# Performance work log

Measured on AMD Instinct MI355X. Metric: run time of the kernel, lower is better.

The kernel has to match this reference:

```python
import jax, jax.numpy as jnp
import numpy as np

B = 8; DIM = 384; H = 8; DH = 48; T = 256; T2 = 64; DEPTH = 4; P = 14; G = 16
SCALE = DIM ** -0.5
BN_INV = 1.0 / float(np.sqrt(1.0 + 1e-5))

def _gelu(x):
    return jax.nn.gelu(x, approximate=False)

def _ln(x, g, b):
    m = x.mean(-1, keepdims=True)
    v = ((x - m) ** 2).mean(-1, keepdims=True)
    return (x - m) / jnp.sqrt(v + 1e-5) * g + b

def _conv(x, w, bi, s, p, groups=1):
    y = jax.lax.conv_general_dilated(x, w, (s, s), [(p, p), (p, p)],
        dimension_numbers=('NCHW', 'OIHW', 'NCHW'), feature_group_count=groups)
    return y + bi[None, :, None, None]

def _gumbel_softmax(logits, key, tau=1.0):
    g = jax.random.gumbel(key, logits.shape, logits.dtype)
    return jax.nn.softmax((logits + g) / tau, axis=-1)

def setup_inputs() -> dict:
    key = jax.random.key(0)
    ks = jax.random.split(key, 20)
    def n(k, shape, s=0.02):
        return jax.random.normal(k, shape, jnp.float32) * s
    D = DEPTH
    return {
        'img': jax.random.normal(ks[0], (B, 3, 224, 224), jnp.float32),
        'adj': jax.random.randint(ks[1], (T, T), 0, 2).astype(jnp.int32),
        'ln_g': jnp.ones((D, DIM), jnp.float32), 'ln_b': jnp.zeros((D, DIM), jnp.float32),
        'gcn_wq': n(ks[2], (D, DH, DH)), 'gcn_wk': n(ks[3], (D, DH, DH)), 'gcn_wv': n(ks[4], (D, DH, DH)),
        'wq': n(ks[5], (D, DIM, DIM)), 'wk': n(ks[6], (D, DIM, DIM)), 'wv': n(ks[7], (D, DIM, DIM)),
        'w_kf': n(ks[8], (D, 2 * DIM, H)), 'w_kf2': n(ks[9], (D, H, T)), 'w_kf3': n(ks[10], (D, H, T2)),
        'sD': jnp.ones((D, H, T), jnp.float32), 'sD2': jnp.ones((D, H, T2), jnp.float32),
        'randmat': n(ks[11], (D, H, H), 1.0),
        'conv1_w': n(ks[12], (DIM, 3, 3, 3), 0.05), 'conv1_b': jnp.zeros((DIM,), jnp.float32),
        'bn_g': jnp.ones((DIM,), jnp.float32), 'bn_b': jnp.zeros((DIM,), jnp.float32),
        'conv2_w': n(ks[13], (DIM, 1, 3, 3), 0.05), 'conv2_b': jnp.zeros((DIM,), jnp.float32),
        'emb_w': n(ks[14], (4 * DIM, DIM)), 'emb_b': jnp.zeros((DIM,), jnp.float32),
        'upool_w': n(ks[15], (DIM, T2)), 'upool_b': jnp.zeros((T2,), jnp.float32),
        'upoolout_w': n(ks[16], (DIM, 1)), 'upoolout_b': jnp.zeros((1,), jnp.float32),
    }

def _forward(img, adj, ln_g, ln_b, gcn_wq, gcn_wk, gcn_wv, wq, wk, wv,
             w_kf, w_kf2, w_kf3, sD, sD2, randmat,
             conv1_w, conv1_b, bn_g, bn_b, conv2_w, conv2_b, emb_w, emb_b,
             upool_w, upool_b, upoolout_w, upoolout_b):
    b = img.shape[0]
    # patchify: (b,3,224,224) -> (b*256, 3, 14, 14)
    x = img.reshape(b, 3, G, P, G, P).transpose(0, 2, 4, 1, 3, 5).reshape(b * G * G, 3, P, P)
    y = _conv(x, conv1_w, conv1_b, 2, 1)                       # (b*256,384,7,7)
    y = y * BN_INV * bn_g[None, :, None, None] + bn_b[None, :, None, None]  # BN eval (mean=0,var=1)
    y = _gelu(y)
    y = _conv(y, conv2_w, conv2_b, 2, 1, groups=DIM)           # depthwise -> (b*256,384,4,4)
    y = y.reshape(b * G * G, DIM, 2, 2, 2, 2).max(axis=(3, 5)) # adaptive max pool -> 2x2
    y = y.reshape(b, G * G, DIM * 4)                           # (b,256, c*p1*p2)
    x = y @ emb_w + emb_b                                      # (b,256,384)
    rep_adj = jnp.broadcast_to(adj.astype(jnp.float32)[None, None], (b, H, T, T))

    def attention(xn, adjbh, i, label):
        t = xn.shape[1]
        x4 = xn.reshape(b, t, H, DH).transpose(0, 2, 1, 3)     # b h t d
        q4 = jnp.einsum('bhts,bhsd->bhtd', adjbh, x4 @ gcn_wq[i])  # GCN: A @ (X W)
        k4 = jnp.einsum('bhts,bhsd->bhtd', adjbh, x4 @ gcn_wk[i])
        q = q4.transpose(0, 2, 1, 3).reshape(b, t, DIM) @ wq[i]
        k = k4.transpose(0, 2, 1, 3).reshape(b, t, DIM) @ wk[i]
        rm0 = _gelu(jnp.concatenate([q, k], -1) @ w_kf[i])     # (b,t,h)
        rm = jnp.einsum('bth,btg->bhg', rm0, rm0)
        if label == 0:
            rmd = jax.nn.sigmoid((rm @ w_kf2[i]) / sD[i])      # (b,h,t)
        else:
            rmd = jax.nn.sigmoid((rm @ w_kf3[i]) / sD2[i])
        qh = q.reshape(b, t, H, DH).transpose(0, 2, 1, 3)
        kh = k.reshape(b, t, H, DH).transpose(0, 2, 1, 3)
        score = jnp.einsum('bhld,bhtd->bhlt', qh, kh) * SCALE
        score = jax.nn.leaky_relu(score)
        score = rmd[:, :, :, None] * score * rmd[:, :, None, :]   # diag_embed(rmd) @ S @ diag_embed(rmd)
        score = jnp.einsum('lh,bhk->blk', randmat[i], score.reshape(b, H, t * t)).reshape(b, H, t, t)
        score = jnp.where(adjbh > 0, score, -1e12)
        attn = jax.nn.softmax(score, axis=-1)
        v4 = jnp.einsum('bhts,bhsd->bhtd', attn, x4 @ gcn_wv[i])  # attn weights as edge weights
        return _gelu(v4.transpose(0, 2, 1, 3).reshape(b, t, DIM) @ wv[i])

    kg = jax.random.key(42)
    for i in range(DEPTH):
        xn = _ln(x, ln_g[i], ln_b[i])
        if i < DEPTH // 2:
            x = attention(xn, rep_adj, i, 0) + x
        else:
            if i == DEPTH // 2:
                tmp = (x @ upool_w + upool_b).transpose(0, 2, 1)       # (b,64,256)
                tmp = _gumbel_softmax(tmp, jax.random.fold_in(kg, i))
                x = tmp @ x                                            # (b,64,384)
                rep_adj = jnp.einsum('bls,bhst->bhlt', tmp, rep_adj)   # C A C^T
                rep_adj = jnp.einsum('bhlt,bmt->bhlm', rep_adj, tmp)
                xn = _ln(x, ln_g[i], ln_b[i])
            x = attention(xn, rep_adj, i, 1) + x

    tmp = (x @ upoolout_w + upoolout_b).transpose(0, 2, 1)             # (b,1,64)
    tmp = _gumbel_softmax(tmp, jax.random.fold_in(kg, 99))
    return tmp @ x                                                     # (b,1,384)

def reference(img, adj, ln_g, ln_b, gcn_wq, gcn_wk, gcn_wv, wq, wk, wv,
              w_kf, w_kf2, w_kf3, sD, sD2, randmat,
              conv1_w, conv1_b, bn_g, bn_b, conv2_w, conv2_b, emb_w, emb_b,
              upool_w, upool_b, upoolout_w, upoolout_b):
    return _forward(img, adj, ln_g, ln_b, gcn_wq, gcn_wk, gcn_wv, wq, wk, wv,
                    w_kf, w_kf2, w_kf3, sD, sD2, randmat,
                    conv1_w, conv1_b, bn_g, bn_b, conv2_w, conv2_b, emb_w, emb_b,
                    upool_w, upool_b, upoolout_w, upoolout_b)
```

## Files before the change

kernel.cpp:

```cpp
#include <hip/hip_runtime.h>
#include <stdint.h>
#include <math.h>

#define NB 8
#define NDIM 384
#define NHD 8
#define DHD 48

__device__ float g_patch[2048 * 1536];
__device__ float g_x[NB * 256 * NDIM];
__device__ float g_xb[NB * 64 * NDIM];
__device__ float g_xq[NB * NHD * 256 * DHD];
__device__ float g_xk[NB * NHD * 256 * DHD];
__device__ float g_xv[NB * NHD * 256 * DHD];
__device__ float g_q4[NB * 256 * NDIM];
__device__ float g_k4[NB * 256 * NDIM];
__device__ float g_q[NB * 256 * NDIM];
__device__ float g_k[NB * 256 * NDIM];
__device__ float g_rm0[NB * 256 * NHD];
__device__ float g_rmd[NB * NHD * 256];
__device__ float g_score[NB * NHD * 256 * 256];
__device__ float g_score2[NB * NHD * 256 * 256];
__device__ float g_logits[NB * 256 * 64];
__device__ float g_tmp[NB * 64 * 256];
__device__ float g_e1[NB * 64 * 256];
__device__ float g_adj2[NB * 64 * 64];

__device__ __forceinline__ float* dev_buf(int s) {
  switch (s) {
    case 0: return g_patch;
    case 1: return g_x;
    case 2: return g_q4;
    case 3: return g_k4;
    case 4: return g_q;
    case 5: return g_k;
    case 6: return g_logits;
    default: return nullptr;
  }
}
#define SEL_PATCH 0
#define SEL_X 1
#define SEL_Q4 2
#define SEL_K4 3
#define SEL_Q 4
#define SEL_K 5
#define SEL_LOGITS 6

__device__ __forceinline__ float gelu_f(float x) {
  return 0.5f * x * (1.0f + erff(x * 0.70710678118654752440f));
}

__host__ __device__ inline void threefry2x32(uint32_t k0, uint32_t k1,
                                             uint32_t x0, uint32_t x1,
                                             uint32_t* o0, uint32_t* o1) {
  uint32_t ks2 = k0 ^ k1 ^ 0x1BD11BDAu;
#define TF_R(r) { x0 += x1; x1 = (x1 << (r)) | (x1 >> (32 - (r))); x1 ^= x0; }
  x0 += k0; x1 += k1;
  TF_R(13) TF_R(15) TF_R(26) TF_R(6)
  x0 += k1; x1 += ks2 + 1u;
  TF_R(17) TF_R(29) TF_R(16) TF_R(24)
  x0 += ks2; x1 += k0 + 2u;
  TF_R(13) TF_R(15) TF_R(26) TF_R(6)
  x0 += k0; x1 += k1 + 3u;
  TF_R(17) TF_R(29) TF_R(16) TF_R(24)
  x0 += k1; x1 += ks2 + 4u;
  TF_R(13) TF_R(15) TF_R(26) TF_R(6)
  x0 += ks2; x1 += k0 + 5u;
#undef TF_R
  *o0 = x0; *o1 = x1;
}

__device__ __forceinline__ double gumbel_from(uint32_t k0, uint32_t k1,
                                              uint32_t idx) {
  uint32_t o0, o1;
  threefry2x32(k0, k1, 0u, idx, &o0, &o1);
  uint32_t bits = o0 ^ o1;
  uint32_t ub = (bits >> 9) | 0x3f800000u;
  float f = __uint_as_float(ub) - 1.0f;
  const float tiny = 1.17549435e-38f;
  float u = fmaxf(f + tiny, tiny);
  return -log(-log((double)u));
}

__global__ __launch_bounds__(256) void k_patch(const float* __restrict__ img,
                                               const float* __restrict__ w1, const float* __restrict__ b1,
                                               const float* __restrict__ bng, const float* __restrict__ bnb,
                                               const float* __restrict__ w2, const float* __restrict__ b2) {
  __shared__ float s_in[3 * 256];
  __shared__ float s_c1[96 * 49];
  __shared__ __align__(16) float s_w1t[27 * 96];
  const float BN_INV = (float)0.99999500003749968752;
  int p = blockIdx.x >> 2;
  int chunk = blockIdx.x & 3;
  int obase = chunk * 96;
  int b = p >> 8, g = p & 255, gi = g >> 4, gj = g & 15;
  int tid = threadIdx.x;
  for (int idx = tid; idx < 3 * 256; idx += 256) {
    int c = idx >> 8, r = idx & 255, py = r >> 4, px = r & 15;
    float v = 0.f;
    if (py >= 1 && py <= 14 && px >= 1 && px <= 14)
      v = img[(((size_t)b * 3 + c) * 224 + gi * 14 + py - 1) * 224 + gj * 14 + px - 1];
    s_in[idx] = v;
  }
  for (int i = tid; i < 27 * 96; i += 256) {
    int j = i / 96, ch = i - j * 96;
    s_w1t[i] = w1[(size_t)(obase + ch) * 27 + j];
  }
  __syncthreads();
  int wave = tid >> 6, lane = tid & 63;
  int y = lane / 7, x = lane - y * 7;
  bool act = lane < 49;
  float in[27];
#pragma unroll
  for (int c = 0; c < 3; ++c)
#pragma unroll
    for (int ky = 0; ky < 3; ++ky)
#pragma unroll
      for (int kx = 0; kx < 3; ++kx)
        in[c * 9 + ky * 3 + kx] = act ? s_in[c * 256 + (2 * y + ky) * 16 + (2 * x + kx)] : 0.f;

  for (int ci = 0; ci < 24; ci += 4) {
    int cl0 = wave * 24 + ci;
    int o0 = obase + cl0;
    float a0 = b1[o0], a1 = b1[o0 + 1], a2 = b1[o0 + 2], a3 = b1[o0 + 3];
#pragma unroll
    for (int j = 0; j < 27; ++j) {
      float4 w = *(const float4*)&s_w1t[j * 96 + cl0];
      float ij = in[j];
      a0 += ij * w.x;
      a1 += ij * w.y;
      a2 += ij * w.z;
      a3 += ij * w.w;
    }
    a0 = a0 * BN_INV * bng[o0] + bnb[o0];
    a1 = a1 * BN_INV * bng[o0 + 1] + bnb[o0 + 1];
    a2 = a2 * BN_INV * bng[o0 + 2] + bnb[o0 + 2];
    a3 = a3 * BN_INV * bng[o0 + 3] + bnb[o0 + 3];
    if (act) {
      s_c1[cl0 * 49 + lane] = gelu_f(a0);
      s_c1[(cl0 + 1) * 49 + lane] = gelu_f(a1);
      s_c1[(cl0 + 2) * 49 + lane] = gelu_f(a2);
      s_c1[(cl0 + 3) * 49 + lane] = gelu_f(a3);
    }
  }
  __syncthreads();
  if (tid < 96) {
    int cl = tid, c = obase + cl;
    float wd[9];
#pragma unroll
    for (int j = 0; j < 9; ++j) wd[j] = w2[c * 9 + j];
    float bb2 = b2[c];
    const float* sc = &s_c1[cl * 49];
    float o2[4][4];
#pragma unroll
    for (int yy = 0; yy < 4; ++yy)
#pragma unroll
      for (int xx = 0; xx < 4; ++xx) {
        float a = bb2;
#pragma unroll
        for (int ky = 0; ky < 3; ++ky) {
          int iy = 2 * yy + ky - 1;
          if (iy < 0 || iy >= 7) continue;
#pragma unroll
          for (int kx = 0; kx < 3; ++kx) {
            int ix = 2 * xx + kx - 1;
            if (ix < 0 || ix >= 7) continue;
            a += sc[iy * 7 + ix] * wd[ky * 3 + kx];
          }
        }
        o2[yy][xx] = a;
      }
    float4 r;
    r.x = fmaxf(fmaxf(o2[0][0], o2[0][1]), fmaxf(o2[1][0], o2[1][1]));
    r.y = fmaxf(fmaxf(o2[0][2], o2[0][3]), fmaxf(o2[1][2], o2[1][3]));
    r.z = fmaxf(fmaxf(o2[2][0], o2[2][1]), fmaxf(o2[3][0], o2[3][1]));
    r.w = fmaxf(fmaxf(o2[2][2], o2[2][3]), fmaxf(o2[3][2], o2[3][3]));
    *(float4*)&g_patch[(size_t)p * 1536 + c * 4] = r;
  }
}

template <int RPB>
__global__ void k_gemm(const float* __restrict__ W, const float* __restrict__ bias,
                       int selA, int selC, int selR,
                       int M, int K, int N, int act) {
  extern __shared__ float sA[];
  const float* A = dev_buf(selA);
  float* C = dev_buf(selC);
  const float* R = (selR >= 0) ? dev_buf(selR) : nullptr;
  int tid = threadIdx.x;
  int bs = blockDim.x;
  int r0 = blockIdx.x * RPB;
  float acc[RPB];
#pragma unroll
  for (int r = 0; r < RPB; ++r) acc[r] = 0.0f;
  const float4 z4 = {0.f, 0.f, 0.f, 0.f};
  for (int k0 = 0; k0 < K; k0 += 384) {
    __syncthreads();
    for (int idx = tid; idx < RPB * 96; idx += bs) {
      int r = idx / 96, q = idx - r * 96;
      int m = r0 + r;
      ((float4*)sA)[idx] = (m < M) ? ((const float4*)(A + (size_t)m * K + k0))[q] : z4;
    }
    __syncthreads();
    const float* Wp = W + (size_t)k0 * N + tid;
    float w0 = Wp[0], w1 = Wp[N], w2 = Wp[2 * (size_t)N], w3 = Wp[3 * (size_t)N];
#pragma unroll 2
    for (int k = 0; k < 384; k += 4) {
      float n0 = 0.f, n1 = 0.f, n2 = 0.f, n3 = 0.f;
      if (k + 4 < 384) {
        const float* Wn = Wp + (size_t)(k + 4) * N;
        n0 = Wn[0]; n1 = Wn[N]; n2 = Wn[2 * (size_t)N]; n3 = Wn[3 * (size_t)N];
      }
#pragma unroll
      for (int r = 0; r < RPB; ++r) {
        float4 a = *(const float4*)&sA[r * 384 + k];
        acc[r] += a.x * w0 + a.y * w1 + a.z * w2 + a.w * w3;
      }
      w0 = n0; w1 = n1; w2 = n2; w3 = n3;
    }
  }
#pragma unroll
  for (int r = 0; r < RPB; ++r) {
    int m = r0 + r;
    if (m >= M) break;
    float v = acc[r];
    if (bias) v += bias[tid];
    if (act == 1) v = gelu_f(v);
    if (R) v += R[(size_t)m * N + tid];
    C[(size_t)m * N + tid] = v;
  }
}

__global__ __launch_bounds__(384) void k_gemm_sk(const float* __restrict__ W, int M, int K, int N) {
  __shared__ float sA[8 * 384];
  int mb = M >> 3;
  int kc = blockIdx.x / mb;
  int rb = blockIdx.x - kc * mb;
  int r0 = rb << 3;
  int k0 = kc * 384;
  int tid = threadIdx.x;
  float acc[8];
#pragma unroll
  for (int r = 0; r < 8; ++r) acc[r] = 0.0f;
  for (int idx = tid; idx < 8 * 96; idx += 384) {
    int r = idx / 96, q = idx - r * 96;
    ((float4*)sA)[idx] = ((const float4*)(g_patch + (size_t)(r0 + r) * K + k0))[q];
  }
  __syncthreads();
  const float* Wp = W + (size_t)k0 * N + tid;
  float w0 = Wp[0], w1 = Wp[N], w2 = Wp[2 * (size_t)N], w3 = Wp[3 * (size_t)N];
#pragma unroll 2
  for (int k = 0; k < 384; k += 4) {
    float n0 = 0.f, n1 = 0.f, n2 = 0.f, n3 = 0.f;
    if (k + 4 < 384) {
      const float* Wn = Wp + (size_t)(k + 4) * N;
      n0 = Wn[0]; n1 = Wn[N]; n2 = Wn[2 * (size_t)N]; n3 = Wn[3 * (size_t)N];
    }
#pragma unroll
    for (int r = 0; r < 8; ++r) {
      float4 a = *(const float4*)&sA[r * 384 + k];
      acc[r] += a.x * w0 + a.y * w1 + a.z * w2 + a.w * w3;
    }
    w0 = n0; w1 = n1; w2 = n2; w3 = n3;
  }
#pragma unroll
  for (int r = 0; r < 8; ++r)
    g_score[((size_t)kc * M + r0 + r) * N + tid] = acc[r];
}

__global__ void k_gemm_skred(const float* __restrict__ bias, int M, int N) {
  int i = blockIdx.x * blockDim.x + threadIdx.x;
  int total = M * N;
  if (i >= total) return;
  size_t stride = (size_t)M * N;
  float v = g_score[i] + g_score[i + stride] + g_score[i + 2 * stride] + g_score[i + 3 * stride];
  g_x[i] = v + bias[i % N];
}

template <int RPB>
__global__ void k_gemmqk(const float* __restrict__ Wq_, const float* __restrict__ Wk_, int M) {
  __shared__ float sA[RPB * 384];
  int half = gridDim.x >> 1;
  bool isK = blockIdx.x >= half;
  int bid = isK ? blockIdx.x - half : blockIdx.x;
  const float* A = isK ? g_k4 : g_q4;
  float* C = isK ? g_k : g_q;
  const float* W = isK ? Wk_ : Wq_;
  const int N = 384;
  int tid = threadIdx.x;
  int r0 = bid * RPB;
  float acc[RPB];
#pragma unroll
  for (int r = 0; r < RPB; ++r) acc[r] = 0.0f;
  for (int idx = tid; idx < RPB * 96; idx += N) {
    int r = idx / 96, q = idx - r * 96;
    ((float4*)sA)[idx] = ((const float4*)(A + (size_t)(r0 + r) * 384))[q];
  }
  __syncthreads();
  const float* Wp = W + tid;
  float w0 = Wp[0], w1 = Wp[N], w2 = Wp[2 * (size_t)N], w3 = Wp[3 * (size_t)N];
#pragma unroll 2
  for (int k = 0; k < 384; k += 4) {
    float n0 = 0.f, n1 = 0.f, n2 = 0.f, n3 = 0.f;
    if (k + 4 < 384) {
      const float* Wn = Wp + (size_t)(k + 4) * N;
      n0 = Wn[0]; n1 = Wn[N]; n2 = Wn[2 * (size_t)N]; n3 = Wn[3 * (size_t)N];
    }
#pragma unroll
    for (int r = 0; r < RPB; ++r) {
      float4 a = *(const float4*)&sA[r * 384 + k];
      acc[r] += a.x * w0 + a.y * w1 + a.z * w2 + a.w * w3;
    }
    w0 = n0; w1 = n1; w2 = n2; w3 = n3;
  }
#pragma unroll
  for (int r = 0; r < RPB; ++r)
    C[(size_t)(r0 + r) * N + tid] = acc[r];
}

__global__ __launch_bounds__(384) void k_lngcn(const float* __restrict__ gg, const float* __restrict__ bb,
                                               const float* __restrict__ Wq, const float* __restrict__ Wk,
                                               const float* __restrict__ Wv, int t) {
  __shared__ float xn[NDIM];
  __shared__ float wred[6];
  int row = blockIdx.x;
  int b = row / t, tt = row - b * t;
  int tid = threadIdx.x;
  int wid = tid >> 6, lane = tid & 63;
  float v = g_x[(size_t)row * NDIM + tid];
  float s = v;
#pragma unroll
  for (int off = 32; off > 0; off >>= 1) s += __shfl_xor(s, off);
  if (lane == 0) wred[wid] = s;
  __syncthreads();
  float tot = wred[0] + wred[1] + wred[2] + wred[3] + wred[4] + wred[5];
  float mean = tot * (1.0f / 384.0f);
  __syncthreads();
  float d = v - mean;
  s = d * d;
#pragma unroll
  for (int off = 32; off > 0; off >>= 1) s += __shfl_xor(s, off);
  if (lane == 0) wred[wid] = s;
  __syncthreads();
  tot = wred[0] + wred[1] + wred[2] + wred[3] + wred[4] + wred[5];
  float var = tot * (1.0f / 384.0f);
  float inv = 1.0f / sqrtf(var + 1e-5f);
  xn[tid] = d * inv * gg[tid] + bb[tid];
  __syncthreads();
  int h = tid / DHD, dd = tid - h * DHD;
  const float* xh = &xn[h * DHD];
  float aq = 0.f, ak = 0.f, av = 0.f;
#pragma unroll 4
  for (int e = 0; e < DHD; ++e) {
    float xv_ = xh[e];
    aq += xv_ * Wq[e * DHD + dd];
    ak += xv_ * Wk[e * DHD + dd];
    av += xv_ * Wv[e * DHD + dd];
  }
  size_t o = ((size_t)(b * NHD + h) * t + tt) * DHD + dd;
  g_xq[o] = aq; g_xk[o] = ak; g_xv[o] = av;
}

__global__ __launch_bounds__(64) void k_adjmm(const int* __restrict__ adji, int use_adj2, int t) {
  __shared__ float arow[8][256];
  int bid = blockIdx.x;
  int nt = t >> 3;
  int lt = bid % nt; int h = (bid / nt) % NHD; int b = bid / (nt * NHD);
  int l0 = lt * 8;
  int tid = threadIdx.x;
  for (int idx = tid; idx < 8 * t; idx += 64) {
    int r = idx / t, s2 = idx - r * t;
    arow[r][s2] = use_adj2 ? g_adj2[((size_t)b * t + l0 + r) * t + s2]
                           : (float)adji[(l0 + r) * 256 + s2];
  }
  __syncthreads();
  if (tid < DHD) {
    const float* xq = g_xq + (size_t)((b * NHD + h) * t) * DHD + tid;
    const float* xk = g_xk + (size_t)((b * NHD + h) * t) * DHD + tid;
    float aq[8] = {0.f, 0.f, 0.f, 0.f, 0.f, 0.f, 0.f, 0.f};
    float ak[8] = {0.f, 0.f, 0.f, 0.f, 0.f, 0.f, 0.f, 0.f};
    for (int s2 = 0; s2 < t; ++s2) {
      float xqv = xq[(size_t)s2 * DHD];
      float xkv = xk[(size_t)s2 * DHD];
#pragma unroll
      for (int r = 0; r < 8; ++r) {
        aq[r] += arow[r][s2] * xqv;
        ak[r] += arow[r][s2] * xkv;
      }
    }
#pragma unroll
    for (int r = 0; r < 8; ++r) {
      size_t o = ((size_t)b * t + l0 + r) * NDIM + h * DHD + tid;
      g_q4[o] = aq[r]; g_k4[o] = ak[r];
    }
  }
}

__global__ __launch_bounds__(64) void k_kf(const float* __restrict__ Wkf) {
  int row = blockIdx.x;
  int tid = threadIdx.x;
  const float* qrow = g_q + (size_t)row * NDIM;
  const float* krow = g_k + (size_t)row * NDIM;
  float accs[8];
#pragma unroll
  for (int j = 0; j < 8; ++j) accs[j] = 0.f;
  for (int m = tid; m < 768; m += 64) {
    float v = (m < 384) ? qrow[m] : krow[m - 384];
    const float* wr = Wkf + (size_t)m * 8;
#pragma unroll
    for (int j = 0; j < 8; ++j) accs[j] += v * wr[j];
  }
#pragma unroll
  for (int j = 0; j < 8; ++j) {
    float a = accs[j];
    for (int off = 32; off > 0; off >>= 1) a += __shfl_xor(a, off);
    if (tid == 0) g_rm0[(size_t)row * 8 + j] = gelu_f(a);
  }
}

__global__ __launch_bounds__(256) void k_rmrmd(const float* __restrict__ Wp,
                                               const float* __restrict__ sDp, int t) {
  __shared__ float red[256];
  __shared__ float rm_s[64];
  int b = blockIdx.x; int tid = threadIdx.x;
  int out = tid & 63, slice = tid >> 6;
  int h = out >> 3, g = out & 7;
  int t4 = t >> 2;
  const float* base = g_rm0 + (size_t)b * t * 8 + (size_t)slice * t4 * 8;
  float acc = 0.f;
  for (int tt = 0; tt < t4; ++tt) acc += base[tt * 8 + h] * base[tt * 8 + g];
  red[slice * 64 + out] = acc;
  __syncthreads();
  if (tid < 64)
    rm_s[tid] = red[tid] + red[64 + tid] + red[128 + tid] + red[192 + tid];
  __syncthreads();
  for (int idx = tid; idx < NHD * t; idx += 256) {
    int s = idx % t; int hh = idx / t;
    const float* rm = rm_s + hh * 8;
    float a = 0.f;
#pragma unroll
    for (int gg = 0; gg < 8; ++gg) a += rm[gg] * Wp[gg * t + s];
    float val = a / sDp[hh * t + s];
    g_rmd[((size_t)(b * NHD + hh)) * t + s] = 1.0f / (1.0f + expf(-val));
  }
}

__global__ void k_score(float scale, int t) {
  __shared__ float qs[8][DHD];
  __shared__ float rl[8];
  int bid = blockIdx.x;
  int nt = t >> 3;
  int lt = bid % nt; int h = (bid / nt) % NHD; int b = bid / (nt * NHD);
  int l0 = lt * 8;
  int tid = threadIdx.x;
  for (int idx = tid; idx < 8 * DHD; idx += t) {
    int r = idx / DHD, d = idx - r * DHD;
    qs[r][d] = g_q[((size_t)b * t + l0 + r) * NDIM + h * DHD + d];
  }
  if (tid < 8) rl[tid] = g_rmd[(size_t)(b * NHD + h) * t + l0 + tid];
  __syncthreads();
  const float* krow = g_k + ((size_t)b * t + tid) * NDIM + h * DHD;
  float4 kr[12];
#pragma unroll
  for (int j = 0; j < 12; ++j) kr[j] = *(const float4*)&krow[j * 4];
  float rmd_s = g_rmd[(size_t)(b * NHD + h) * t + tid];
#pragma unroll
  for (int r = 0; r < 8; ++r) {
    float acc = 0.f;
#pragma unroll
    for (int j = 0; j < 12; ++j) {
      float4 qq = *(const float4*)&qs[r][j * 4];
      acc += kr[j].x * qq.x + kr[j].y * qq.y + kr[j].z * qq.z + kr[j].w * qq.w;
    }
    float v = acc * scale;
    v = (v >= 0.f) ? v : 0.01f * v;
    v = rl[r] * v * rmd_s;
    g_score[((size_t)(b * NHD + h) * t + l0 + r) * t + tid] = v;
  }
}

template <int T>
__global__ void k_mix8(const float* __restrict__ RM, const int* __restrict__ adji,
                       int use_adj2) {
  __shared__ float p[8][T];
  __shared__ float rmat[64];
  int bid = blockIdx.x;
  int l = bid % T, b = bid / T;
  int tt = threadIdx.x;
  if (tt < 64) rmat[tt] = RM[tt];
  __syncthreads();
  float sv[8];
#pragma unroll
  for (int h = 0; h < 8; ++h)
    sv[h] = g_score[((size_t)(b * NHD + h) * T + l) * T + tt];
  bool m = use_adj2 ? (g_adj2[((size_t)b * T + l) * T + tt] > 0.f)
                    : (adji[l * 256 + tt] > 0);
#pragma unroll
  for (int g = 0; g < 8; ++g) {
    float a = 0.f;
#pragma unroll
    for (int h = 0; h < 8; ++h) a += rmat[g * 8 + h] * sv[h];
    p[g][tt] = m ? a : -1e12f;
  }
  __syncthreads();
  int wid = tt >> 6, lane = tt & 63;
  const int NW = T / 64;
  const int RPW = 8 / NW;
  const int EPL = T / 64;
  for (int rr = 0; rr < RPW; ++rr) {
    int row = wid * RPW + rr;
    float mv = -1e30f;
#pragma unroll
    for (int e = 0; e < EPL; ++e) mv = fmaxf(mv, p[row][lane + e * 64]);
#pragma unroll
    for (int off = 32; off > 0; off >>= 1) mv = fmaxf(mv, __shfl_xor(mv, off));
    float sum = 0.f;
#pragma unroll
    for (int e = 0; e < EPL; ++e) {
      float ev = expf(p[row][lane + e * 64] - mv);
      p[row][lane + e * 64] = ev;
      sum += ev;
    }
#pragma unroll
    for (int off = 32; off > 0; off >>= 1) sum += __shfl_xor(sum, off);
    float inv = 1.0f / sum;
#pragma unroll
    for (int e = 0; e < EPL; ++e) p[row][lane + e * 64] *= inv;
  }
  __syncthreads();
#pragma unroll
  for (int h = 0; h < 8; ++h)
    g_score2[((size_t)(b * NHD + h) * T + l) * T + tt] = p[h][tt];
}

__global__ __launch_bounds__(64) void k_attnv(int t) {
  __shared__ float arow[8][256];
  int bid = blockIdx.x;
  int nt = t >> 3;
  int lt = bid % nt; int h = (bid / nt) % NHD; int b = bid / (nt * NHD);
  int l0 = lt * 8;
  int tid = threadIdx.x;
  for (int idx = tid; idx < 8 * t; idx += 64) {
    int r = idx / t, s2 = idx - r * t;
    arow[r][s2] = g_score2[((size_t)(b * NHD + h) * t + l0 + r) * t + s2];
  }
  __syncthreads();
  if (tid < DHD) {
    const float* xv = g_xv + (size_t)((b * NHD + h) * t) * DHD + tid;
    float acc[8] = {0.f, 0.f, 0.f, 0.f, 0.f, 0.f, 0.f, 0.f};
    for (int s2 = 0; s2 < t; ++s2) {
      float xvv = xv[(size_t)s2 * DHD];
#pragma unroll
      for (int r = 0; r < 8; ++r) acc[r] += arow[r][s2] * xvv;
    }
#pragma unroll
    for (int r = 0; r < 8; ++r)
      g_q4[((size_t)b * t + l0 + r) * NDIM + h * DHD + tid] = acc[r];
  }
}

__global__ __launch_bounds__(256) void k_gumbel_pool(uint32_t k0, uint32_t k1) {
  __shared__ double red2[256];
  int bj = blockIdx.x;
  int b = bj >> 6, j = bj & 63;
  int tt = threadIdx.x;
  uint32_t n = (uint32_t)bj * 256u + (uint32_t)tt;
  double gum = gumbel_from(k0, k1, n);
  double val = (double)g_logits[((size_t)b * 256 + tt) * 64 + j] + gum;
  red2[tt] = val; __syncthreads();
  for (int s = 128; s > 0; s >>= 1) { if (tt < s) red2[tt] = fmax(red2[tt], red2[tt + s]); __syncthreads(); }
  double mx = red2[0]; __syncthreads();
  double e = exp(val - mx);
  red2[tt] = e; __syncthreads();
  for (int s = 128; s > 0; s >>= 1) { if (tt < s) red2[tt] += red2[tt + s]; __syncthreads(); }
  g_tmp[(size_t)bj * 256 + tt] = (float)(e / red2[0]);
}

__global__ __launch_bounds__(384) void k_poolx() {
  __shared__ float trow[256];
  int bj = blockIdx.x; int b = bj >> 6;
  int tid = threadIdx.x;
  if (tid < 256) trow[tid] = g_tmp[(size_t)bj * 256 + tid];
  __syncthreads();
  float acc = 0.f;
  const float* xb = g_x + (size_t)b * 256 * NDIM + tid;
  for (int tt = 0; tt < 256; ++tt) acc += trow[tt] * xb[(size_t)tt * NDIM];
  g_xb[(size_t)bj * NDIM + tid] = acc;
}

__global__ void k_copyx(int n) {
  int i = blockIdx.x * blockDim.x + threadIdx.x;
  if (i < n) g_x[i] = g_xb[i];
}

__global__ __launch_bounds__(256) void k_pooladj1(const int* __restrict__ adji) {
  __shared__ float trow[256];
  int bl = blockIdx.x;
  int tid = threadIdx.x;
  trow[tid] = g_tmp[(size_t)bl * 256 + tid];
  __syncthreads();
  float acc = 0.f;
  for (int s = 0; s < 256; ++s) acc += trow[s] * (float)adji[s * 256 + tid];
  g_e1[(size_t)bl * 256 + tid] = acc;
}

__global__ __launch_bounds__(64) void k_pooladj2() {
  __shared__ float erow[256];
  int bl = blockIdx.x; int b = bl >> 6;
  int tid = threadIdx.x;
  for (int s = tid; s < 256; s += 64) erow[s] = g_e1[(size_t)bl * 256 + s];
  __syncthreads();
  const float* tm = g_tmp + ((size_t)b * 64 + tid) * 256;
  float acc = 0.f;
  for (int s = 0; s < 256; ++s) acc += erow[s] * tm[s];
  g_adj2[(size_t)bl * 64 + tid] = acc;
}

__global__ __launch_bounds__(384) void k_final(const float* __restrict__ w, const float* __restrict__ bias,
                                               uint32_t k0, uint32_t k1, float* __restrict__ out) {
  __shared__ double sv[64];
  __shared__ double sp[64];
  int b = blockIdx.x;
  int tid = threadIdx.x;
  if (tid < 256) {
    int gq = tid >> 2, l4 = tid & 3;
    const float* x = g_x + (size_t)(b * 64 + gq) * NDIM;
    float acc = 0.f;
    for (int c = l4; c < NDIM; c += 4) acc += x[c] * w[c];
    acc += __shfl_xor(acc, 1, 4);
    acc += __shfl_xor(acc, 2, 4);
    if (l4 == 0) {
      float lg = acc + bias[0];
      sv[gq] = (double)lg + gumbel_from(k0, k1, (uint32_t)(b * 64 + gq));
    }
  }
  __syncthreads();
  double mx = -1e30;
  for (int i2 = 0; i2 < 64; ++i2) mx = fmax(mx, sv[i2]);
  if (tid < 64) sp[tid] = exp(sv[tid] - mx);
  __syncthreads();
  double sum = 0.;
  for (int i2 = 0; i2 < 64; ++i2) sum += sp[i2];
  float acc = 0.f;
  const float* xb = g_x + (size_t)b * 64 * NDIM + tid;
  for (int tt = 0; tt < 64; ++tt) acc += (float)(sp[tt] / sum) * xb[(size_t)tt * NDIM];
  out[(size_t)b * NDIM + tid] = acc;
}

extern "C" void kernel_launch(void* const* d_in, const int* in_sizes, int n_in,
                              void* d_out, int out_size, void* d_ws, size_t ws_size,
                              hipStream_t stream) {
  const float* img = (const float*)d_in[0];
  const int* adj = (const int*)d_in[1];
  const float* ln_g = (const float*)d_in[2];
  const float* ln_b = (const float*)d_in[3];
  const float* gcn_wq = (const float*)d_in[4];
  const float* gcn_wk = (const float*)d_in[5];
  const float* gcn_wv = (const float*)d_in[6];
  const float* wq = (const float*)d_in[7];
  const float* wk = (const float*)d_in[8];
  const float* wv = (const float*)d_in[9];
  const float* w_kf = (const float*)d_in[10];
  const float* w_kf2 = (const float*)d_in[11];
  const float* w_kf3 = (const float*)d_in[12];
  const float* sD = (const float*)d_in[13];
  const float* sD2 = (const float*)d_in[14];
  const float* randmat = (const float*)d_in[15];
  const float* conv1_w = (const float*)d_in[16];
  const float* conv1_b = (const float*)d_in[17];
  const float* bn_g = (const float*)d_in[18];
  const float* bn_b = (const float*)d_in[19];
  const float* conv2_w = (const float*)d_in[20];
  const float* conv2_b = (const float*)d_in[21];
  const float* emb_w = (const float*)d_in[22];
  const float* emb_b = (const float*)d_in[23];
  const float* upool_w = (const float*)d_in[24];
  const float* upool_b = (const float*)d_in[25];
  const float* upoolout_w = (const float*)d_in[26];
  const float* upoolout_b = (const float*)d_in[27];
  float* out = (float*)d_out;

  uint32_t k2a, k2b, k99a, k99b;
  threefry2x32(0u, 42u, 0u, 2u, &k2a, &k2b);
  threefry2x32(0u, 42u, 0u, 99u, &k99a, &k99b);

  const float SCALE = (float)(1.0 / sqrt(384.0));

  k_patch<<<2048 * 4, 256, 0, stream>>>(img, conv1_w, conv1_b, bn_g, bn_b, conv2_w, conv2_b);
  k_gemm_sk<<<1024, 384, 0, stream>>>(emb_w, 2048, 1536, 384);
  k_gemm_skred<<<(2048 * 384 + 255) / 256, 256, 0, stream>>>(emb_b, 2048, 384);

  auto attention = [&](int i, int t, int label) {
    int rows = NB * t;
    int bht8 = NB * NHD * t / 8;
    int use_adj2 = (t == 64) ? 1 : 0;
    k_lngcn<<<rows, 384, 0, stream>>>(ln_g + i * 384, ln_b + i * 384,
                                      gcn_wq + i * 2304, gcn_wk + i * 2304,
                                      gcn_wv + i * 2304, t);
    k_adjmm<<<bht8, 64, 0, stream>>>(adj, use_adj2, t);
    if (rows == 2048) {
      k_gemmqk<4><<<1024, 384, 0, stream>>>(wq + i * 147456, wk + i * 147456, rows);
    } else {
      k_gemmqk<2><<<512, 384, 0, stream>>>(wq + i * 147456, wk + i * 147456, rows);
    }
    k_kf<<<rows, 64, 0, stream>>>(w_kf + i * 6144);
    const float* Wp = label ? (w_kf3 + i * 512) : (w_kf2 + i * 2048);
    const float* sDp = label ? (sD2 + i * 512) : (sD + i * 2048);
    k_rmrmd<<<NB, 256, 0, stream>>>(Wp, sDp, t);
    k_score<<<bht8, t, 0, stream>>>(SCALE, t);
    if (t == 256) {
      k_mix8<256><<<rows, 256, 0, stream>>>(randmat + i * 64, adj, use_adj2);
    } else {
      k_mix8<64><<<rows, 64, 0, stream>>>(randmat + i * 64, adj, use_adj2);
    }
    k_attnv<<<bht8, 64, 0, stream>>>(t);
    if (rows == 2048) {
      k_gemm<4><<<512, 384, 4 * 384 * sizeof(float), stream>>>(
          wv + i * 147456, nullptr, SEL_Q4, SEL_X, SEL_X, rows, 384, 384, 1);
    } else {
      k_gemm<2><<<256, 384, 2 * 384 * sizeof(float), stream>>>(
          wv + i * 147456, nullptr, SEL_Q4, SEL_X, SEL_X, rows, 384, 384, 1);
    }
  };

  attention(0, 256, 0);
  attention(1, 256, 0);

  k_gemm<2><<<1024, 64, 2 * 384 * sizeof(float), stream>>>(
      upool_w, upool_b, SEL_X, SEL_LOGITS, -1, 2048, 384, 64, 0);
  k_gumbel_pool<<<512, 256, 0, stream>>>(k2a, k2b);
  k_poolx<<<512, 384, 0, stream>>>();
  k_copyx<<<(NB * 64 * NDIM + 255) / 256, 256, 0, stream>>>(NB * 64 * NDIM);
  k_pooladj1<<<512, 256, 0, stream>>>(adj);
  k_pooladj2<<<512, 64, 0, stream>>>();

  attention(2, 64, 1);
  attention(3, 64, 1);

  k_final<<<8, 384, 0, stream>>>(upoolout_w, upoolout_b, k99a, k99b, out);
}
```

Before: 898.1 us.

## Fuse pooling kernels and T=64 attention into single kernels, drop x copy

For the pooled stage (T=64), one k_attn64 kernel now computes scores, the randmat head mix, the adjacency mask, softmax and attention-times-V per row. This replaces the separate k_score, k_mix8 and k_attnv launches and their global score buffers. The gumbel softmax is merged with x pooling, and the two adjacency-pooling matmuls share one kernel. The copy of g_xb back into g_x is removed by having later stages read g_xb through a selector. The aim is fewer launches and less global round-trip traffic, at the cost of low parallelism in the fused kernels (64-thread blocks with serial loops).

```diff
diff --git a/kernel.cpp b/kernel.cpp
--- a/kernel.cpp
+++ b/kernel.cpp
@@ -23,7 +23,6 @@
 __device__ float g_score2[NB * NHD * 256 * 256];
 __device__ float g_logits[NB * 256 * 64];
 __device__ float g_tmp[NB * 64 * 256];
-__device__ float g_e1[NB * 64 * 256];
 __device__ float g_adj2[NB * 64 * 64];
 
 __device__ __forceinline__ float* dev_buf(int s) {
@@ -35,6 +34,7 @@
     case 4: return g_q;
     case 5: return g_k;
     case 6: return g_logits;
+    case 7: return g_xb;
     default: return nullptr;
   }
 }
@@ -45,6 +45,7 @@
 #define SEL_Q 4
 #define SEL_K 5
 #define SEL_LOGITS 6
+#define SEL_XB 7
 
 __device__ __forceinline__ float gelu_f(float x) {
   return 0.5f * x * (1.0f + erff(x * 0.70710678118654752440f));
@@ -320,14 +321,15 @@
 
 __global__ __launch_bounds__(384) void k_lngcn(const float* __restrict__ gg, const float* __restrict__ bb,
                                                const float* __restrict__ Wq, const float* __restrict__ Wk,
-                                               const float* __restrict__ Wv, int t) {
+                                               const float* __restrict__ Wv, int t, int selX) {
   __shared__ float xn[NDIM];
   __shared__ float wred[6];
+  const float* X = dev_buf(selX);
   int row = blockIdx.x;
   int b = row / t, tt = row - b * t;
   int tid = threadIdx.x;
   int wid = tid >> 6, lane = tid & 63;
-  float v = g_x[(size_t)row * NDIM + tid];
+  float v = X[(size_t)row * NDIM + tid];
   float s = v;
 #pragma unroll
   for (int off = 32; off > 0; off >>= 1) s += __shfl_xor(s, off);
@@ -559,61 +561,123 @@
   }
 }
 
-__global__ __launch_bounds__(256) void k_gumbel_pool(uint32_t k0, uint32_t k1) {
+__global__ __launch_bounds__(64) void k_attn64(const float* __restrict__ RM, float scale) {
+  const int T = 64;
+  __shared__ float qs[NDIM];
+  __shared__ float rmat[64];
+  __shared__ float rl[8];
+  __shared__ float p[8][64];
+  __shared__ float res[16];
+  int bid = blockIdx.x;
+  int l = bid % T, b = bid / T;
+  int tt = threadIdx.x;
+  for (int i = tt; i < NDIM; i += T) qs[i] = g_q[((size_t)b * T + l) * NDIM + i];
+  rmat[tt] = RM[tt];
+  if (tt < 8) rl[tt] = g_rmd[((size_t)(b * NHD + tt)) * T + l];
+  __syncthreads();
+  const float* krow = g_k + ((size_t)b * T + tt) * NDIM;
+  float s[8];
+#pragma unroll
+  for (int h = 0; h < 8; ++h) {
+    float acc = 0.f;
+#pragma unroll
+    for (int j = 0; j < 12; ++j) {
+      float4 kk = *(const float4*)&krow[h * DHD + j * 4];
+      float4 qq = *(const float4*)&qs[h * DHD + j * 4];
+      acc += kk.x * qq.x + kk.y * qq.y + kk.z * qq.z + kk.w * qq.w;
+    }
+    float v = acc * scale;
+    v = (v >= 0.f) ? v : 0.01f * v;
+    s[h] = rl[h] * v * g_rmd[((size_t)(b * NHD + h)) * T + tt];
+  }
+  bool m = g_adj2[((size_t)b * T + l) * T + tt] > 0.f;
+  float sv[8];
+#pragma unroll
+  for (int g = 0; g < 8; ++g) {
+    float a = 0.f;
+#pragma unroll
+    for (int h = 0; h < 8; ++h) a += rmat[g * 8 + h] * s[h];
+    sv[g] = m ? a : -1e12f;
+    p[g][tt] = sv[g];
+  }
+  __syncthreads();
+  int g = tt >> 3, j = tt & 7;
+  float mval = -1e30f;
+  for (int i = j; i < T; i += 8) mval = fmaxf(mval, p[g][i]);
+#pragma unroll
+  for (int off = 4; off > 0; off >>= 1) mval = fmaxf(mval, __shfl_xor(mval, off, 8));
+  if (j == 0) res[g] = mval;
+  __syncthreads();
+#pragma unroll
+  for (int g2 = 0; g2 < 8; ++g2) p[g2][tt] = expf(sv[g2] - res[g2]);
+  __syncthreads();
+  float sval = 0.f;
+  for (int i = j; i < T; i += 8) sval += p[g][i];
+#pragma unroll
+  for (int off = 4; off > 0; off >>= 1) sval += __shfl_xor(sval, off, 8);
+  if (j == 0) res[8 + g] = sval;
+  __syncthreads();
+  for (int o = tt; o < NDIM; o += T) {
+    int gg = o / DHD, dd = o - gg * DHD;
+    const float* xv = g_xv + ((size_t)(b * NHD + gg) * T) * DHD + dd;
+    const float* pa = p[gg];
+    float acc = 0.f;
+#pragma unroll 4
+    for (int s2 = 0; s2 < T; ++s2) acc += pa[s2] * xv[(size_t)s2 * DHD];
+    g_q4[((size_t)b * T + l) * NDIM + o] = acc / res[8 + gg];
+  }
+}
+
+__global__ __launch_bounds__(384) void k_gpoolx(uint32_t k0, uint32_t k1) {
   __shared__ double red2[256];
+  __shared__ float trow[256];
   int bj = blockIdx.x;
   int b = bj >> 6, j = bj & 63;
   int tt = threadIdx.x;
-  uint32_t n = (uint32_t)bj * 256u + (uint32_t)tt;
-  double gum = gumbel_from(k0, k1, n);
-  double val = (double)g_logits[((size_t)b * 256 + tt) * 64 + j] + gum;
-  red2[tt] = val; __syncthreads();
+  double val = 0.;
+  if (tt < 256) {
+    uint32_t n = (uint32_t)bj * 256u + (uint32_t)tt;
+    val = (double)g_logits[((size_t)b * 256 + tt) * 64 + j] + gumbel_from(k0, k1, n);
+    red2[tt] = val;
+  }
+  __syncthreads();
   for (int s = 128; s > 0; s >>= 1) { if (tt < s) red2[tt] = fmax(red2[tt], red2[tt + s]); __syncthreads(); }
-  double mx = red2[0]; __syncthreads();
-  double e = exp(val - mx);
-  red2[tt] = e; __syncthreads();
+  double mx = red2[0];
+  __syncthreads();
+  double e = 0.;
+  if (tt < 256) { e = exp(val - mx); red2[tt] = e; }
+  __syncthreads();
   for (int s = 128; s > 0; s >>= 1) { if (tt < s) red2[tt] += red2[tt + s]; __syncthreads(); }
-  g_tmp[(size_t)bj * 256 + tt] = (float)(e / red2[0]);
-}
-
-__global__ __launch_bounds__(384) void k_poolx() {
+  if (tt < 256) {
+    float tv = (float)(e / red2[0]);
+    trow[tt] = tv;
+    g_tmp[(size_t)bj * 256 + tt] = tv;
+  }
+  __syncthreads();
+  float acc = 0.f;
+  const float* xb = g_x + (size_t)b * 256 * NDIM + tt;
+  for (int s2 = 0; s2 < 256; ++s2) acc += trow[s2] * xb[(size_t)s2 * NDIM];
+  g_xb[(size_t)bj * NDIM + tt] = acc;
+}
+
+__global__ __launch_bounds__(256) void k_pooladj(const int* __restrict__ adji) {
   __shared__ float trow[256];
-  int bj = blockIdx.x; int b = bj >> 6;
-  int tid = threadIdx.x;
-  if (tid < 256) trow[tid] = g_tmp[(size_t)bj * 256 + tid];
-  __syncthreads();
-  float acc = 0.f;
-  const float* xb = g_x + (size_t)b * 256 * NDIM + tid;
-  for (int tt = 0; tt < 256; ++tt) acc += trow[tt] * xb[(size_t)tt * NDIM];
-  g_xb[(size_t)bj * NDIM + tid] = acc;
-}
-
-__global__ void k_copyx(int n) {
-  int i = blockIdx.x * blockDim.x + threadIdx.x;
-  if (i < n) g_x[i] = g_xb[i];
-}
-
-__global__ __launch_bounds__(256) void k_pooladj1(const int* __restrict__ adji) {
-  __shared__ float trow[256];
+  __shared__ float erow[256];
   int bl = blockIdx.x;
+  int b = bl >> 6;
   int tid = threadIdx.x;
   trow[tid] = g_tmp[(size_t)bl * 256 + tid];
   __syncthreads();
   float acc = 0.f;
   for (int s = 0; s < 256; ++s) acc += trow[s] * (float)adji[s * 256 + tid];
-  g_e1[(size_t)bl * 256 + tid] = acc;
-}
-
-__global__ __launch_bounds__(64) void k_pooladj2() {
-  __shared__ float erow[256];
-  int bl = blockIdx.x; int b = bl >> 6;
-  int tid = threadIdx.x;
-  for (int s = tid; s < 256; s += 64) erow[s] = g_e1[(size_t)bl * 256 + s];
-  __syncthreads();
-  const float* tm = g_tmp + ((size_t)b * 64 + tid) * 256;
-  float acc = 0.f;
-  for (int s = 0; s < 256; ++s) acc += erow[s] * tm[s];
-  g_adj2[(size_t)bl * 64 + tid] = acc;
+  erow[tid] = acc;
+  __syncthreads();
+  if (tid < 64) {
+    const float* tm = g_tmp + ((size_t)b * 64 + tid) * 256;
+    float a2 = 0.f;
+    for (int s = 0; s < 256; ++s) a2 += erow[s] * tm[s];
+    g_adj2[(size_t)bl * 64 + tid] = a2;
+  }
 }
 
 __global__ __launch_bounds__(384) void k_final(const float* __restrict__ w, const float* __restrict__ bias,
@@ -624,7 +688,7 @@
   int tid = threadIdx.x;
   if (tid < 256) {
     int gq = tid >> 2, l4 = tid & 3;
-    const float* x = g_x + (size_t)(b * 64 + gq) * NDIM;
+    const float* x = g_xb + (size_t)(b * 64 + gq) * NDIM;
     float acc = 0.f;
     for (int c = l4; c < NDIM; c += 4) acc += x[c] * w[c];
     acc += __shfl_xor(acc, 1, 4);
@@ -642,7 +706,7 @@
   double sum = 0.;
   for (int i2 = 0; i2 < 64; ++i2) sum += sp[i2];
   float acc = 0.f;
-  const float* xb = g_x + (size_t)b * 64 * NDIM + tid;
+  const float* xb = g_xb + (size_t)b * 64 * NDIM + tid;
   for (int tt = 0; tt < 64; ++tt) acc += (float)(sp[tt] / sum) * xb[(size_t)tt * NDIM];
   out[(size_t)b * NDIM + tid] = acc;
 }
@@ -690,13 +754,13 @@
   k_gemm_sk<<<1024, 384, 0, stream>>>(emb_w, 2048, 1536, 384);
   k_gemm_skred<<<(2048 * 384 + 255) / 256, 256, 0, stream>>>(emb_b, 2048, 384);
 
-  auto attention = [&](int i, int t, int label) {
+  auto attention = [&](int i, int t, int label, int selx) {
     int rows = NB * t;
     int bht8 = NB * NHD * t / 8;
     int use_adj2 = (t == 64) ? 1 : 0;
     k_lngcn<<<rows, 384, 0, stream>>>(ln_g + i * 384, ln_b + i * 384,
                                       gcn_wq + i * 2304, gcn_wk + i * 2304,
-                                      gcn_wv + i * 2304, t);
+                                      gcn_wv + i * 2304, t, selx);
     k_adjmm<<<bht8, 64, 0, stream>>>(adj, use_adj2, t);
     if (rows == 2048) {
       k_gemmqk<4><<<1024, 384, 0, stream>>>(wq + i * 147456, wk + i * 147456, rows);
@@ -707,35 +771,32 @@
     const float* Wp = label ? (w_kf3 + i * 512) : (w_kf2 + i * 2048);
     const float* sDp = label ? (sD2 + i * 512) : (sD + i * 2048);
     k_rmrmd<<<NB, 256, 0, stream>>>(Wp, sDp, t);
-    k_score<<<bht8, t, 0, stream>>>(SCALE, t);
     if (t == 256) {
+      k_score<<<bht8, t, 0, stream>>>(SCALE, t);
       k_mix8<256><<<rows, 256, 0, stream>>>(randmat + i * 64, adj, use_adj2);
+      k_attnv<<<bht8, 64, 0, stream>>>(t);
     } else {
-      k_mix8<64><<<rows, 64, 0, stream>>>(randmat + i * 64, adj, use_adj2);
-    }
-    k_attnv<<<bht8, 64, 0, stream>>>(t);
+      k_attn64<<<rows, 64, 0, stream>>>(randmat + i * 64, SCALE);
+    }
     if (rows == 2048) {
       k_gemm<4><<<512, 384, 4 * 384 * sizeof(float), stream>>>(
-          wv + i * 147456, nullptr, SEL_Q4, SEL_X, SEL_X, rows, 384, 384, 1);
+          wv + i * 147456, nullptr, SEL_Q4, selx, selx, rows, 384, 384, 1);
     } else {
       k_gemm<2><<<256, 384, 2 * 384 * sizeof(float), stream>>>(
-          wv + i * 147456, nullptr, SEL_Q4, SEL_X, SEL_X, rows, 384, 384, 1);
+          wv + i * 147456, nullptr, SEL_Q4, selx, selx, rows, 384, 384, 1);
     }
   };
 
-  attention(0, 256, 0);
-  attention(1, 256, 0);
+  attention(0, 256, 0, SEL_X);
+  attention(1, 256, 0, SEL_X);
 
   k_gemm<2><<<1024, 64, 2 * 384 * sizeof(float), stream>>>(
       upool_w, upool_b, SEL_X, SEL_LOGITS, -1, 2048, 384, 64, 0);
-  k_gumbel_pool<<<512, 256, 0, stream>>>(k2a, k2b);
-  k_poolx<<<512, 384, 0, stream>>>();
-  k_copyx<<<(NB * 64 * NDIM + 255) / 256, 256, 0, stream>>>(NB * 64 * NDIM);
-  k_pooladj1<<<512, 256, 0, stream>>>(adj);
-  k_pooladj2<<<512, 64, 0, stream>>>();
-
-  attention(2, 64, 1);
-  attention(3, 64, 1);
+  k_gpoolx<<<512, 384, 0, stream>>>(k2a, k2b);
+  k_pooladj<<<512, 256, 0, stream>>>(adj);
+
+  attention(2, 64, 1, SEL_XB);
+  attention(3, 64, 1, SEL_XB);
 
   k_final<<<8, 384, 0, stream>>>(upoolout_w, upoolout_b, k99a, k99b, out);
 }
```

Result: slower. 933.2 us (+3.9%).
